# Kernel optimization log

Hardware: AMD Instinct MI355X
Metric: run time of the kernel (lower is better)

## Reference

```python
import jax, jax.numpy as jnp
from jax import lax
import numpy as np

B, S, V, E, H = 256, 1024, 288, 100, 128


def setup_inputs() -> dict:
    key = jax.random.key(0)
    ks = jax.random.split(key, 16)
    d = {
        "text": jax.random.randint(ks[0], (B, S), 0, V, dtype=jnp.int32),
        "emb": jax.random.normal(ks[1], (V, E), jnp.float32) * 0.1,
        "fcW": jax.random.normal(ks[2], (V, H), jnp.float32) * 0.1,
        "fcb": jax.random.normal(ks[3], (V,), jnp.float32) * 0.1,
    }
    in_dims = [E, H, H]
    for l in range(3):
        kk = jax.random.split(ks[4 + l], 4)
        d[f"Wih{l}"] = jax.random.normal(kk[0], (4 * H, in_dims[l]), jnp.float32) * 0.1
        d[f"Whh{l}"] = jax.random.normal(kk[1], (4 * H, H), jnp.float32) * 0.1
        d[f"bih{l}"] = jax.random.normal(kk[2], (4 * H,), jnp.float32) * 0.1
        d[f"bhh{l}"] = jax.random.normal(kk[3], (4 * H,), jnp.float32) * 0.1
    return d


def _lstm_layer(x, Wih, Whh, bih, bhh):
    # x: [S, B, in]; PyTorch gate order i, f, g, o
    xg = jnp.einsum('sbe,ge->sbg', x, Wih) + (bih + bhh)  # precompute input proj [S,B,4H]
    Hh = Whh.shape[1]
    WhhT = Whh.T

    def step(carry, xg_t):
        h, c = carry
        g = xg_t + h @ WhhT
        i, f, gg, o = jnp.split(g, 4, axis=-1)
        c = jax.nn.sigmoid(f) * c + jax.nn.sigmoid(i) * jnp.tanh(gg)
        h = jax.nn.sigmoid(o) * jnp.tanh(c)
        return (h, c), h

    b = x.shape[1]
    init = (jnp.zeros((b, Hh), x.dtype), jnp.zeros((b, Hh), x.dtype))
    _, hs = lax.scan(step, init, xg)
    return hs  # [S, B, H]


def reference(text, emb, Wih0, Whh0, bih0, bhh0, Wih1, Whh1, bih1, bhh1,
              Wih2, Whh2, bih2, bhh2, fcW, fcb):
    # embedding (dropout is identity in eval mode)
    x = emb[text]                  # [B, S, E]
    x = jnp.transpose(x, (1, 0, 2))  # time-major [S, B, E]
    x = _lstm_layer(x, Wih0, Whh0, bih0, bhh0)
    x = _lstm_layer(x, Wih1, Whh1, bih1, bhh1)
    x = _lstm_layer(x, Wih2, Whh2, bih2, bhh2)
    # fc head; original returns prediction.transpose(0,1) -> [S, B, V]
    pred = jnp.einsum('sbh,vh->sbv', x, fcW) + fcb
    return pred
```

## Files before the change

kernel.cpp:

```cpp
#include <hip/hip_runtime.h>
#include <cstddef>
#include <cstdint>

#define BB 256
#define SS 1024
#define VV 288
#define EE 100
#define HH 128
#define G4 512
#define CH 16
#define NCH (SS / CH)

typedef _Float16 half8 __attribute__((ext_vector_type(8)));
typedef float f32x4 __attribute__((ext_vector_type(4)));

__device__ __forceinline__ float sig_f(float x) {
    return __builtin_amdgcn_rcpf(1.0f +
           __builtin_amdgcn_exp2f(-1.4426950408889634f * x));
}
__device__ __forceinline__ float tanh2_f(float x) {
    return 2.0f * __builtin_amdgcn_rcpf(1.0f +
           __builtin_amdgcn_exp2f(-2.8853900817779268f * x)) - 1.0f;
}

__global__ __launch_bounds__(512) void proj_kernel(
    const float* __restrict__ emb, const float* __restrict__ Wih0,
    const float* __restrict__ bih0, const float* __restrict__ bhh0,
    float* __restrict__ table)
{
    __shared__ float er[EE];
    const int v = blockIdx.x;
    const int j = threadIdx.x;
    for (int e = j; e < EE; e += 512) er[e] = emb[v * EE + e];
    __syncthreads();
    float acc = bih0[j] + bhh0[j];
    const float* wr = Wih0 + j * EE;
#pragma unroll 4
    for (int e = 0; e < EE; e++) acc = fmaf(er[e], wr[e], acc);
    table[v * G4 + j] = acc;
}

__global__ __launch_bounds__(256) void pack_fc(
    const float* __restrict__ W, _Float16* __restrict__ out)
{
    const int tid = blockIdx.x * 256 + threadIdx.x;
    const int e  = tid & 7;
    const int l  = (tid >> 3) & 63;
    const int f  = tid >> 9;
    const int kc = f & 3, nt = f >> 2;
    const int n = nt * 16 + (l & 15);
    const int k = kc * 32 + (l >> 4) * 8 + e;
    out[tid] = (_Float16)W[n * HH + k];
}

__global__ __launch_bounds__(512)
__attribute__((amdgpu_waves_per_eu(2, 2)))
void lstm_pipe(const int* __restrict__ text, const float* __restrict__ table,
               const float* Whh0f,
               const float* Wih1f, const float* Whh1f,
               const float* __restrict__ bih1, const float* __restrict__ bhh1,
               const float* Wih2f, const float* Whh2f,
               const float* __restrict__ bih2, const float* __restrict__ bhh2,
               _Float16* hX, _Float16* hY, int* prog)
{
    __shared__ int tokL[SS * 16];
    __shared__ _Float16 Hb[2][2048];
    const int tid = threadIdx.x;
    const int w = tid >> 6, l = tid & 63;
    const int layer = blockIdx.x >> 4;
    const int bt = blockIdx.x & 15;
    const int B0 = bt * 16;
    const int colD = l & 15, qd = l >> 4;
    const int gcol = w * 16 + colD;

    const float* WhhF = (layer == 0) ? Whh0f : ((layer == 1) ? Whh1f : Whh2f);
    const float* WihF = (layer == 2) ? Wih2f : Wih1f;
    const float* bihp = (layer == 2) ? bih2 : bih1;
    const float* bhhp = (layer == 2) ? bhh2 : bhh1;
    const _Float16* xin = (layer == 1) ? hX : hY;
    _Float16* hout = (layer == 1) ? hY : hX;
    int* prog_src = prog + (layer - 1) * 16 + bt;
    int* prog_my  = prog + layer * 16 + bt;

    half8 whh[4][4], wih[4][4];
#pragma unroll
    for (int gt = 0; gt < 4; gt++)
#pragma unroll
        for (int kc = 0; kc < 4; kc++) {
            const int n = gt * 128 + gcol;
            const int k0 = kc * 32 + qd * 8;
            const float4 a0 = *(const float4*)(WhhF + (size_t)n * HH + k0);
            const float4 a1 = *(const float4*)(WhhF + (size_t)n * HH + k0 + 4);
            half8 hf;
            hf[0] = (_Float16)a0.x; hf[1] = (_Float16)a0.y;
            hf[2] = (_Float16)a0.z; hf[3] = (_Float16)a0.w;
            hf[4] = (_Float16)a1.x; hf[5] = (_Float16)a1.y;
            hf[6] = (_Float16)a1.z; hf[7] = (_Float16)a1.w;
            whh[gt][kc] = hf;
            if (layer) {
                const float4 b0 = *(const float4*)(WihF + (size_t)n * HH + k0);
                const float4 b1 = *(const float4*)(WihF + (size_t)n * HH + k0 + 4);
                half8 hg;
                hg[0] = (_Float16)b0.x; hg[1] = (_Float16)b0.y;
                hg[2] = (_Float16)b0.z; hg[3] = (_Float16)b0.w;
                hg[4] = (_Float16)b1.x; hg[5] = (_Float16)b1.y;
                hg[6] = (_Float16)b1.z; hg[7] = (_Float16)b1.w;
                wih[gt][kc] = hg;
            }
        }
    f32x4 bias_frag[4];
#pragma unroll
    for (int gt = 0; gt < 4; gt++) {
        float b = 0.0f;
        if (layer) {
            const int g = gt * 128 + gcol;
            b = bihp[g] + bhhp[g];
        }
        bias_frag[gt] = (f32x4){b, b, b, b};
    }
    if (layer == 0) {
        for (int kk = 0; kk < 32; kk++) {
            const int lin = kk * 512 + tid;
            const int b = lin >> 10, t = lin & 1023;
            tokL[t * 16 + b] = text[(((size_t)B0 + b) << 10) | t];
        }
    }
    for (int i = tid; i < 2048; i += 512) Hb[0][i] = (_Float16)0.0f;
    f32x4 c_acc = {0.f, 0.f, 0.f, 0.f};

    int rd_idx[4], wr_idx[4];
#pragma unroll
    for (int kc = 0; kc < 4; kc++)
        rd_idx[kc] = (colD * 128 + kc * 32 + qd * 8) ^ ((colD & 7) << 3);
#pragma unroll
    for (int r = 0; r < 4; r++) {
        const int rr = 4 * qd + r;
        wr_idx[r] = (rr * 128 + gcol) ^ ((rr & 7) << 3);
    }
    _Float16* houtp = hout + ((size_t)B0 + 4 * qd) * HH + gcol;
    __syncthreads();

    auto wait_src = [&](int target) {
        int v = __hip_atomic_load(prog_src, __ATOMIC_RELAXED,
                                  __HIP_MEMORY_SCOPE_AGENT);
        while (v < target) {
            __builtin_amdgcn_s_sleep(8);
            v = __hip_atomic_load(prog_src, __ATOMIC_RELAXED,
                                  __HIP_MEMORY_SCOPE_AGENT);
        }
        v = __hip_atomic_load(prog_src, __ATOMIC_ACQUIRE,
                              __HIP_MEMORY_SCOPE_AGENT);
        asm volatile("" :: "v"(v));
    };
    auto signal = [&](int c) {
        asm volatile("s_waitcnt vmcnt(0)" ::: "memory");
        __builtin_amdgcn_s_barrier();
        if (tid == 0) {
            __threadfence();
            __hip_atomic_store(prog_my, (c + 1) * CH, __ATOMIC_RELEASE,
                               __HIP_MEMORY_SCOPE_AGENT);
        }
    };
    auto finish = [&](f32x4 (&p)[4], f32x4 (&q)[4], int nxt) {
#pragma unroll
        for (int r = 0; r < 4; r++) {
            const float gi = p[0][r] + q[0][r];
            const float gf = p[1][r] + q[1][r];
            const float gg = p[2][r] + q[2][r];
            const float go = p[3][r] + q[3][r];
            const float si = sig_f(gi);
            const float sf = sig_f(gf);
            const float tg = tanh2_f(gg);
            const float so = sig_f(go);
            const float cc = fmaf(sf, c_acc[r], si * tg);
            c_acc[r] = cc;
            const float hv = so * tanh2_f(cc);
            const _Float16 hh = (_Float16)hv;
            Hb[nxt][wr_idx[r]] = hh;
            houtp[r * HH] = hh;
        }
        houtp += BB * HH;
        asm volatile("s_waitcnt lgkmcnt(0)" ::: "memory");
        __builtin_amdgcn_s_barrier();
    };

    if (layer == 0) {
        f32x4 xgA[4], xgB[4];
        {
            const int4 tk0 = *(const int4*)&tokL[4 * qd];
            const float* g0 = table + (size_t)tk0.x * G4 + gcol;
            const float* g1 = table + (size_t)tk0.y * G4 + gcol;
            const float* g2 = table + (size_t)tk0.z * G4 + gcol;
            const float* g3 = table + (size_t)tk0.w * G4 + gcol;
#pragma unroll
            for (int gt = 0; gt < 4; gt++) {
                xgA[gt][0] = g0[gt * 128];
                xgA[gt][1] = g1[gt * 128];
                xgA[gt][2] = g2[gt * 128];
                xgA[gt][3] = g3[gt * 128];
            }
        }
        auto step0 = [&](int T, int cur, f32x4 (&xgc)[4], f32x4 (&xgn)[4]) {
            half8 a_h[4];
#pragma unroll
            for (int kc = 0; kc < 4; kc++)
                a_h[kc] = *(const half8*)&Hb[cur][rd_idx[kc]];
            const int Tn = (T + 1 < SS) ? T + 1 : T;
            const int4 tkn = *(const int4*)&tokL[Tn * 16 + 4 * qd];
            f32x4 p[4], q[4];
#pragma unroll
            for (int gt = 0; gt < 4; gt++) {
                f32x4 t = __builtin_amdgcn_mfma_f32_16x16x32_f16(
                    a_h[0], whh[gt][0], xgc[gt], 0, 0, 0);
                p[gt] = __builtin_amdgcn_mfma_f32_16x16x32_f16(
                    a_h[1], whh[gt][1], t, 0, 0, 0);
                f32x4 u = __builtin_amdgcn_mfma_f32_16x16x32_f16(
                    a_h[2], whh[gt][2], (f32x4){0.f, 0.f, 0.f, 0.f}, 0, 0, 0);
                q[gt] = __builtin_amdgcn_mfma_f32_16x16x32_f16(
                    a_h[3], whh[gt][3], u, 0, 0, 0);
            }
            {
                const float* g0 = table + (size_t)tkn.x * G4 + gcol;
                const float* g1 = table + (size_t)tkn.y * G4 + gcol;
                const float* g2 = table + (size_t)tkn.z * G4 + gcol;
                const float* g3 = table + (size_t)tkn.w * G4 + gcol;
#pragma unroll
                for (int gt = 0; gt < 4; gt++) {
                    xgn[gt][0] = g0[gt * 128];
                    xgn[gt][1] = g1[gt * 128];
                    xgn[gt][2] = g2[gt * 128];
                    xgn[gt][3] = g3[gt * 128];
                }
            }
            finish(p, q, cur ^ 1);
        };
        for (int c = 0; c < NCH; c++) {
            for (int tt = 0; tt < CH; tt += 2) {
                step0(c * CH + tt,     0, xgA, xgB);
                step0(c * CH + tt + 1, 1, xgB, xgA);
            }
            signal(c);
        }
    } else {
        wait_src(2 * CH);
        const _Float16* xbase = xin + ((size_t)B0 + colD) * HH + qd * 8;
        half8 xcur[4];
        f32x4 accXA[4], accXB[4];
#pragma unroll
        for (int kc = 0; kc < 4; kc++)
            xcur[kc] = *(const half8*)(xbase + (size_t)0 * BB * HH + kc * 32);
#pragma unroll
        for (int gt = 0; gt < 4; gt++) {
            f32x4 t = bias_frag[gt];
#pragma unroll
            for (int kc = 0; kc < 4; kc++)
                t = __builtin_amdgcn_mfma_f32_16x16x32_f16(
                    xcur[kc], wih[gt][kc], t, 0, 0, 0);
            accXA[gt] = t;
        }
#pragma unroll
        for (int kc = 0; kc < 4; kc++)
            xcur[kc] = *(const half8*)(xbase + (size_t)1 * BB * HH + kc * 32);

        auto stepK = [&](int T, int cur, f32x4 (&accXc)[4], f32x4 (&accXn)[4]) {
            half8 a_h[4];
#pragma unroll
            for (int kc = 0; kc < 4; kc++)
                a_h[kc] = *(const half8*)&Hb[cur][rd_idx[kc]];
            f32x4 p[4], q[4];
#pragma unroll
            for (int gt = 0; gt < 4; gt++) {
                f32x4 t = __builtin_amdgcn_mfma_f32_16x16x32_f16(
                    a_h[0], whh[gt][0], accXc[gt], 0, 0, 0);
                p[gt] = __builtin_amdgcn_mfma_f32_16x16x32_f16(
                    a_h[1], whh[gt][1], t, 0, 0, 0);
                f32x4 u = __builtin_amdgcn_mfma_f32_16x16x32_f16(
                    a_h[2], whh[gt][2], (f32x4){0.f, 0.f, 0.f, 0.f}, 0, 0, 0);
                q[gt] = __builtin_amdgcn_mfma_f32_16x16x32_f16(
                    a_h[3], whh[gt][3], u, 0, 0, 0);
            }
#pragma unroll
            for (int gt = 0; gt < 4; gt++) {
                f32x4 t = bias_frag[gt];
#pragma unroll
                for (int kc = 0; kc < 4; kc++)
                    t = __builtin_amdgcn_mfma_f32_16x16x32_f16(
                        xcur[kc], wih[gt][kc], t, 0, 0, 0);
                accXn[gt] = t;
            }
            {
                const size_t tf =
                    (T + 2 < SS) ? (size_t)(T + 2) : (size_t)(SS - 1);
#pragma unroll
                for (int kc = 0; kc < 4; kc++)
                    xcur[kc] = *(const half8*)(xbase + tf * BB * HH + kc * 32);
            }
            finish(p, q, cur ^ 1);
        };
        for (int c = 0; c < NCH; c++) {
            if (c) {
                const int tgt = (c + 2) * CH;
                wait_src(tgt > SS ? SS : tgt);
            }
            for (int tt = 0; tt < CH; tt += 2) {
                stepK(c * CH + tt,     0, accXA, accXB);
                stepK(c * CH + tt + 1, 1, accXB, accXA);
            }
            if (layer == 1) signal(c);
        }
    }
}

__global__ __launch_bounds__(256) void fc_mfma(
    const _Float16* __restrict__ h2, const _Float16* __restrict__ pfcW,
    const float* __restrict__ fcb, float* __restrict__ out)
{
    const int tid = threadIdx.x, wv = tid >> 6, l = tid & 63;
    const int colD = l & 15, qd = l >> 4;
    const size_t m0 = (size_t)blockIdx.x * 64 + wv * 16;
    half8 a[4];
#pragma unroll
    for (int kc = 0; kc < 4; kc++)
        a[kc] = *(const half8*)(h2 + (m0 + colD) * HH + kc * 32 + qd * 8);
    float fcb_r[18];
#pragma unroll
    for (int nt = 0; nt < 18; nt++) fcb_r[nt] = fcb[nt * 16 + colD];
#pragma unroll
    for (int nt = 0; nt < 18; nt++) {
        f32x4 acc = {0.f, 0.f, 0.f, 0.f};
#pragma unroll
        for (int kc = 0; kc < 4; kc++) {
            const half8 b = *(const half8*)(pfcW + (((nt * 4 + kc) << 6) + l) * 8);
            acc = __builtin_amdgcn_mfma_f32_16x16x32_f16(a[kc], b, acc, 0, 0, 0);
        }
#pragma unroll
        for (int r = 0; r < 4; r++)
            out[(m0 + 4 * qd + r) * VV + nt * 16 + colD] = acc[r] + fcb_r[nt];
    }
}

extern "C" void kernel_launch(void* const* d_in, const int* in_sizes, int n_in,
                              void* d_out, int out_size, void* d_ws, size_t ws_size,
                              hipStream_t stream)
{
    (void)in_sizes; (void)n_in; (void)ws_size;
    const int*   text = (const int*)  d_in[0];
    const float* emb  = (const float*)d_in[1];
    const float* fcW  = (const float*)d_in[2];
    const float* fcb  = (const float*)d_in[3];
    const float* Wih0 = (const float*)d_in[4];
    const float* Whh0 = (const float*)d_in[5];
    const float* bih0 = (const float*)d_in[6];
    const float* bhh0 = (const float*)d_in[7];
    const float* Wih1 = (const float*)d_in[8];
    const float* Whh1 = (const float*)d_in[9];
    const float* bih1 = (const float*)d_in[10];
    const float* bhh1 = (const float*)d_in[11];
    const float* Wih2 = (const float*)d_in[12];
    const float* Whh2 = (const float*)d_in[13];
    const float* bih2 = (const float*)d_in[14];
    const float* bhh2 = (const float*)d_in[15];
    float* out = (float*)d_out;

    float* table = (float*)d_ws;
    _Float16* hX = (_Float16*)((char*)d_ws + 589824);
    _Float16* hY = hX + (size_t)SS * BB * HH;
    _Float16* pfcW = (_Float16*)d_ws;
    int* prog = ((int*)d_out) + ((size_t)out_size - 64);

    hipMemsetAsync(prog, 0, 64 * sizeof(int), stream);
    proj_kernel<<<VV, 512, 0, stream>>>(emb, Wih0, bih0, bhh0, table);
    lstm_pipe<<<48, 512, 0, stream>>>(text, table, Whh0,
                                      Wih1, Whh1, bih1, bhh1,
                                      Wih2, Whh2, bih2, bhh2,
                                      hX, hY, prog);
    pack_fc<<<144, 256, 0, stream>>>(fcW, pfcW);
    fc_mfma<<<4096, 256, 0, stream>>>(hX, pfcW, fcb, out);
}
```

Before: 1.603 ms.

## Pack LSTM gate math into float2 pairs and merge reciprocals; reorder MFMA chain

```diff
diff --git a/kernel.cpp b/kernel.cpp
--- a/kernel.cpp
+++ b/kernel.cpp
@@ -13,14 +13,42 @@
 
 typedef _Float16 half8 __attribute__((ext_vector_type(8)));
 typedef float f32x4 __attribute__((ext_vector_type(4)));
-
-__device__ __forceinline__ float sig_f(float x) {
-    return __builtin_amdgcn_rcpf(1.0f +
-           __builtin_amdgcn_exp2f(-1.4426950408889634f * x));
-}
-__device__ __forceinline__ float tanh2_f(float x) {
-    return 2.0f * __builtin_amdgcn_rcpf(1.0f +
-           __builtin_amdgcn_exp2f(-2.8853900817779268f * x)) - 1.0f;
+typedef float f32x2 __attribute__((ext_vector_type(2)));
+
+__device__ __forceinline__ f32x2 exp2_2(f32x2 a) {
+    f32x2 r;
+    r[0] = __builtin_amdgcn_exp2f(a[0]);
+    r[1] = __builtin_amdgcn_exp2f(a[1]);
+    return r;
+}
+__device__ __forceinline__ f32x2 rcp_2(f32x2 a) {
+    f32x2 r;
+    r[0] = __builtin_amdgcn_rcpf(a[0]);
+    r[1] = __builtin_amdgcn_rcpf(a[1]);
+    return r;
+}
+__device__ __forceinline__ f32x2 vmin2(f32x2 a, float m) {
+    f32x2 r;
+    r[0] = fminf(a[0], m);
+    r[1] = fminf(a[1], m);
+    return r;
+}
+
+__device__ __forceinline__ f32x2 lstm_pair(
+    f32x2 gi, f32x2 gf, f32x2 gg, f32x2 go, f32x2& cc)
+{
+    const float L1 = -1.4426950408889634f;
+    const float L2 = -2.8853900817779268f;
+    const f32x2 one = {1.0f, 1.0f};
+    f32x2 ai = exp2_2(gi * L1);
+    f32x2 bg = exp2_2(vmin2(gg * L2, 80.0f));
+    f32x2 af = exp2_2(gf * L1);
+    f32x2 sf = rcp_2(af + one);
+    f32x2 it = (one - bg) * rcp_2((ai + one) * (bg + one));
+    cc = __builtin_elementwise_fma(sf, cc, it);
+    f32x2 dc = exp2_2(vmin2(cc * L2, 80.0f));
+    f32x2 ao = exp2_2(go * L1);
+    return (one - dc) * rcp_2((ao + one) * (dc + one));
 }
 
 __global__ __launch_bounds__(512) void proj_kernel(
@@ -126,7 +154,7 @@
         }
     }
     for (int i = tid; i < 2048; i += 512) Hb[0][i] = (_Float16)0.0f;
-    f32x4 c_acc = {0.f, 0.f, 0.f, 0.f};
+    f32x2 c_acc0 = {0.f, 0.f}, c_acc1 = {0.f, 0.f};
 
     int rd_idx[4], wr_idx[4];
 #pragma unroll
@@ -161,23 +189,32 @@
                                __HIP_MEMORY_SCOPE_AGENT);
         }
     };
-    auto finish = [&](f32x4 (&p)[4], f32x4 (&q)[4], int nxt) {
-#pragma unroll
-        for (int r = 0; r < 4; r++) {
-            const float gi = p[0][r] + q[0][r];
-            const float gf = p[1][r] + q[1][r];
-            const float gg = p[2][r] + q[2][r];
-            const float go = p[3][r] + q[3][r];
-            const float si = sig_f(gi);
-            const float sf = sig_f(gf);
-            const float tg = tanh2_f(gg);
-            const float so = sig_f(go);
-            const float cc = fmaf(sf, c_acc[r], si * tg);
-            c_acc[r] = cc;
-            const float hv = so * tanh2_f(cc);
-            const _Float16 hh = (_Float16)hv;
-            Hb[nxt][wr_idx[r]] = hh;
-            houtp[r * HH] = hh;
+    auto finish = [&](f32x4 (&acc)[4], int nxt) {
+        {
+            f32x2 gi = {acc[0][0], acc[0][1]};
+            f32x2 gf = {acc[1][0], acc[1][1]};
+            f32x2 gg = {acc[2][0], acc[2][1]};
+            f32x2 go = {acc[3][0], acc[3][1]};
+            f32x2 hv = lstm_pair(gi, gf, gg, go, c_acc0);
+            const _Float16 h0 = (_Float16)hv[0];
+            const _Float16 h1 = (_Float16)hv[1];
+            Hb[nxt][wr_idx[0]] = h0;
+            Hb[nxt][wr_idx[1]] = h1;
+            houtp[0 * HH] = h0;
+            houtp[1 * HH] = h1;
+        }
+        {
+            f32x2 gi = {acc[0][2], acc[0][3]};
+            f32x2 gf = {acc[1][2], acc[1][3]};
+            f32x2 gg = {acc[2][2], acc[2][3]};
+            f32x2 go = {acc[3][2], acc[3][3]};
+            f32x2 hv = lstm_pair(gi, gf, gg, go, c_acc1);
+            const _Float16 h2 = (_Float16)hv[0];
+            const _Float16 h3 = (_Float16)hv[1];
+            Hb[nxt][wr_idx[2]] = h2;
+            Hb[nxt][wr_idx[3]] = h3;
+            houtp[2 * HH] = h2;
+            houtp[3 * HH] = h3;
         }
         houtp += BB * HH;
         asm volatile("s_waitcnt lgkmcnt(0)" ::: "memory");
@@ -205,21 +242,9 @@
 #pragma unroll
             for (int kc = 0; kc < 4; kc++)
                 a_h[kc] = *(const half8*)&Hb[cur][rd_idx[kc]];
-            const int Tn = (T + 1 < SS) ? T + 1 : T;
-            const int4 tkn = *(const int4*)&tokL[Tn * 16 + 4 * qd];
-            f32x4 p[4], q[4];
-#pragma unroll
-            for (int gt = 0; gt < 4; gt++) {
-                f32x4 t = __builtin_amdgcn_mfma_f32_16x16x32_f16(
-                    a_h[0], whh[gt][0], xgc[gt], 0, 0, 0);
-                p[gt] = __builtin_amdgcn_mfma_f32_16x16x32_f16(
-                    a_h[1], whh[gt][1], t, 0, 0, 0);
-                f32x4 u = __builtin_amdgcn_mfma_f32_16x16x32_f16(
-                    a_h[2], whh[gt][2], (f32x4){0.f, 0.f, 0.f, 0.f}, 0, 0, 0);
-                q[gt] = __builtin_amdgcn_mfma_f32_16x16x32_f16(
-                    a_h[3], whh[gt][3], u, 0, 0, 0);
-            }
             {
+                const int Tn = (T + 1 < SS) ? T + 1 : T;
+                const int4 tkn = *(const int4*)&tokL[Tn * 16 + 4 * qd];
                 const float* g0 = table + (size_t)tkn.x * G4 + gcol;
                 const float* g1 = table + (size_t)tkn.y * G4 + gcol;
                 const float* g2 = table + (size_t)tkn.z * G4 + gcol;
@@ -232,7 +257,17 @@
                     xgn[gt][3] = g3[gt * 128];
                 }
             }
-            finish(p, q, cur ^ 1);
+            f32x4 acc[4];
+#pragma unroll
+            for (int gt = 0; gt < 4; gt++) {
+                f32x4 t = xgc[gt];
+#pragma unroll
+                for (int kc = 0; kc < 4; kc++)
+                    t = __builtin_amdgcn_mfma_f32_16x16x32_f16(
+                        a_h[kc], whh[gt][kc], t, 0, 0, 0);
+                acc[gt] = t;
+            }
+            finish(acc, cur ^ 1);
         };
         for (int c = 0; c < NCH; c++) {
             for (int tt = 0; tt < CH; tt += 2) {
@@ -267,18 +302,6 @@
 #pragma unroll
             for (int kc = 0; kc < 4; kc++)
                 a_h[kc] = *(const half8*)&Hb[cur][rd_idx[kc]];
-            f32x4 p[4], q[4];
-#pragma unroll
-            for (int gt = 0; gt < 4; gt++) {
-                f32x4 t = __builtin_amdgcn_mfma_f32_16x16x32_f16(
-                    a_h[0], whh[gt][0], accXc[gt], 0, 0, 0);
-                p[gt] = __builtin_amdgcn_mfma_f32_16x16x32_f16(
-                    a_h[1], whh[gt][1], t, 0, 0, 0);
-                f32x4 u = __builtin_amdgcn_mfma_f32_16x16x32_f16(
-                    a_h[2], whh[gt][2], (f32x4){0.f, 0.f, 0.f, 0.f}, 0, 0, 0);
-                q[gt] = __builtin_amdgcn_mfma_f32_16x16x32_f16(
-                    a_h[3], whh[gt][3], u, 0, 0, 0);
-            }
 #pragma unroll
             for (int gt = 0; gt < 4; gt++) {
                 f32x4 t = bias_frag[gt];
@@ -295,7 +318,17 @@
                 for (int kc = 0; kc < 4; kc++)
                     xcur[kc] = *(const half8*)(xbase + tf * BB * HH + kc * 32);
             }
-            finish(p, q, cur ^ 1);
+            f32x4 acc[4];
+#pragma unroll
+            for (int gt = 0; gt < 4; gt++) {
+                f32x4 t = accXc[gt];
+#pragma unroll
+                for (int kc = 0; kc < 4; kc++)
+                    t = __builtin_amdgcn_mfma_f32_16x16x32_f16(
+                        a_h[kc], whh[gt][kc], t, 0, 0, 0);
+                acc[gt] = t;
+            }
+            finish(acc, cur ^ 1);
         };
         for (int c = 0; c < NCH; c++) {
             if (c) {
```

After: 1.728 ms. +7.8%, slower.
